# Kernel tuning notes

Measured on AMD Instinct MI355X. Metric: run time of the kernel, lower is better.

Reference implementation:

```python
import jax, jax.numpy as jnp
import numpy as np

B, N_ELEM, N_NODES, E2 = 4096, 2048, 1024, 4096


def setup_inputs() -> dict:
    key = jax.random.key(0)
    k = jax.random.split(key, 7)
    return {
        "EA": jax.random.normal(k[0], (B, N_ELEM), dtype=jnp.float32),
        "e": jax.random.normal(k[1], (B, N_ELEM), dtype=jnp.float32),
        "q": jax.random.normal(k[2], (B, N_NODES, 2), dtype=jnp.float32),
        "r": jax.random.normal(k[3], (B, N_NODES, 2), dtype=jnp.float32),
        "vecs": jax.random.normal(k[4], (E2, 2), dtype=jnp.float32),
        "node_ids": jax.random.randint(k[5], (E2,), 0, N_NODES, dtype=jnp.int32),
        "elem_ids": jax.random.randint(k[6], (E2,), 0, N_ELEM, dtype=jnp.int32),
    }


def reference(EA, e, q, r, vecs, node_ids, elem_ids):
    # axial_forces = EA * e : [B, N_ELEM]
    axial = EA * e
    # gather per incidence entry and scale by the 2-vector: [B, E2, 2]
    contrib = axial[:, elem_ids][..., None] * vecs[None, :, :]
    n_sample, n_nodes = q.shape[0], q.shape[1]
    # scatter-add contributions into per-node residual: [B, N_NODES, 2]
    residual = jnp.zeros((n_sample, n_nodes, 2), dtype=EA.dtype)
    residual = residual.at[:, node_ids, :].add(contrib)
    residual = residual - q - r
    return jnp.mean(jnp.square(residual))
```

## Files before the change

kernel.cpp:

```cpp
#include <hip/hip_runtime.h>

#define B_SAMPLES 4096
#define N_ELEM    2048
#define N_NODES   1024
#define E2        4096
#define BLOCK     256
#define SLOTS     32
#define S         4
#define MAIN_BLOCKS (B_SAMPLES / S)

#define WS_CNT_OFF   0
#define WS_ELL_OFF   4096
#define WS_PART_OFF  (4096 + SLOTS * N_NODES * 16)

__global__ __launch_bounds__(BLOCK) void neq_zero_kernel(
    float4* __restrict__ ell, int* __restrict__ cnt)
{
    const int i = blockIdx.x * BLOCK + threadIdx.x;
    ell[i] = make_float4(0.f, 0.f, 0.f, 0.f);
    if (i < N_NODES) cnt[i] = 0;
}

__global__ __launch_bounds__(BLOCK) void neq_build_kernel(
    const float* __restrict__ vecs, const int* __restrict__ node_ids,
    const int* __restrict__ elem_ids, int* __restrict__ cnt,
    float4* __restrict__ ell)
{
    const int j = blockIdx.x * BLOCK + threadIdx.x;
    int nid = node_ids[j];
    int eid = elem_ids[j];
    float2 v = ((const float2*)vecs)[j];
    int slot = atomicAdd(&cnt[nid], 1);
    if (slot < SLOTS) {
        ell[slot * N_NODES + nid] = make_float4(v.x, v.y, __int_as_float(eid), 0.f);
    }
}

__global__ __launch_bounds__(BLOCK, 4) void neq_main_kernel(
    const float* __restrict__ EA, const float* __restrict__ e,
    const float* __restrict__ q,  const float* __restrict__ r,
    const int* __restrict__ cnt, const float4* __restrict__ ell,
    float* __restrict__ partial)
{
    __shared__ float4 axial4[N_ELEM];
    __shared__ float red[BLOCK / 64];

    const int b0 = blockIdx.x * S;
    const int t = threadIdx.x;

#pragma unroll
    for (int i = 0; i < N_ELEM / BLOCK; ++i) {
        int eid = t + i * BLOCK;
        float4 p;
        const float* EAp = EA + (size_t)b0 * N_ELEM + eid;
        const float* ep  = e  + (size_t)b0 * N_ELEM + eid;
        p.x = EAp[0 * N_ELEM] * ep[0 * N_ELEM];
        p.y = EAp[1 * N_ELEM] * ep[1 * N_ELEM];
        p.z = EAp[2 * N_ELEM] * ep[2 * N_ELEM];
        p.w = EAp[3 * N_ELEM] * ep[3 * N_ELEM];
        axial4[eid] = p;
    }

    int c0 = min(cnt[t], SLOTS);
    int c1 = min(cnt[t + 256], SLOTS);
    int c2 = min(cnt[t + 512], SLOTS);
    int c3 = min(cnt[t + 768], SLOTS);
    int kmax = max(max(c0, c1), max(c2, c3));
    __syncthreads();

    float accx[4][S] = {};
    float accy[4][S] = {};
    for (int k = 0; k < kmax; ++k) {
        const float4* row = ell + k * N_NODES + t;
#pragma unroll
        for (int i = 0; i < 4; ++i) {
            float4 pk = row[i * BLOCK];
            int eid = __float_as_int(pk.z);
            float4 ax = axial4[eid];
            accx[i][0] += ax.x * pk.x;  accy[i][0] += ax.x * pk.y;
            accx[i][1] += ax.y * pk.x;  accy[i][1] += ax.y * pk.y;
            accx[i][2] += ax.z * pk.x;  accy[i][2] += ax.z * pk.y;
            accx[i][3] += ax.w * pk.x;  accy[i][3] += ax.w * pk.y;
        }
    }

    float acc = 0.f;
#pragma unroll
    for (int s = 0; s < S; ++s) {
        const float2* q2 = (const float2*)(q + (size_t)(b0 + s) * N_NODES * 2);
        const float2* r2 = (const float2*)(r + (size_t)(b0 + s) * N_NODES * 2);
#pragma unroll
        for (int i = 0; i < 4; ++i) {
            int n = t + i * BLOCK;
            float2 qv = q2[n];
            float2 rv = r2[n];
            float x = accx[i][s] - qv.x - rv.x;
            float y = accy[i][s] - qv.y - rv.y;
            acc += x * x + y * y;
        }
    }

#pragma unroll
    for (int off = 32; off > 0; off >>= 1)
        acc += __shfl_down(acc, off, 64);
    if ((t & 63) == 0) red[t >> 6] = acc;
    __syncthreads();
    if (t == 0) partial[blockIdx.x] = red[0] + red[1] + red[2] + red[3];
}

__global__ __launch_bounds__(1024) void neq_reduce_kernel(
    const float* __restrict__ partial, float* __restrict__ out)
{
    __shared__ float red[1024 / 64];
    const int t = threadIdx.x;
    float acc = partial[t];
#pragma unroll
    for (int off = 32; off > 0; off >>= 1)
        acc += __shfl_down(acc, off, 64);
    if ((t & 63) == 0) red[t >> 6] = acc;
    __syncthreads();
    if (t == 0) {
        float s = 0.f;
#pragma unroll
        for (int w = 0; w < 1024 / 64; ++w) s += red[w];
        const float inv_n = 1.0f / (float)((size_t)B_SAMPLES * N_NODES * 2);
        out[0] = s * inv_n;
    }
}

extern "C" void kernel_launch(void* const* d_in, const int* in_sizes, int n_in,
                              void* d_out, int out_size, void* d_ws, size_t ws_size,
                              hipStream_t stream) {
    const float* EA       = (const float*)d_in[0];
    const float* e        = (const float*)d_in[1];
    const float* q        = (const float*)d_in[2];
    const float* r        = (const float*)d_in[3];
    const float* vecs     = (const float*)d_in[4];
    const int*   node_ids = (const int*)d_in[5];
    const int*   elem_ids = (const int*)d_in[6];

    char* ws = (char*)d_ws;
    int*    cnt     = (int*)(ws + WS_CNT_OFF);
    float4* ell     = (float4*)(ws + WS_ELL_OFF);
    float*  partial = (float*)(ws + WS_PART_OFF);

    neq_zero_kernel<<<(SLOTS * N_NODES) / BLOCK, BLOCK, 0, stream>>>(ell, cnt);
    neq_build_kernel<<<E2 / BLOCK, BLOCK, 0, stream>>>(
        vecs, node_ids, elem_ids, cnt, ell);
    neq_main_kernel<<<MAIN_BLOCKS, BLOCK, 0, stream>>>(
        EA, e, q, r, cnt, ell, partial);
    neq_reduce_kernel<<<1, 1024, 0, stream>>>(partial, (float*)d_out);
}
```

Measured before the change: 162.4 us.

## Prefetch q/r and ELL rows early, fold final reduction into atomicAdd

Loads q and r and sums them before the scatter loop so their global latency overlaps the ELL traversal. The ELL loop becomes software-pipelined, fetching the next slot row while the current one is processed. The separate single-block reduce kernel is removed: each main block atomically adds its scaled partial into the output, which is zeroed by a memset. This saves a launch and a dependent tail kernel, at the cost of extra registers and a float atomic whose ordering makes the result nondeterministic.

```diff
diff --git a/kernel.cpp b/kernel.cpp
--- a/kernel.cpp
+++ b/kernel.cpp
@@ -11,7 +11,6 @@
 
 #define WS_CNT_OFF   0
 #define WS_ELL_OFF   4096
-#define WS_PART_OFF  (4096 + SLOTS * N_NODES * 16)
 
 __global__ __launch_bounds__(BLOCK) void neq_zero_kernel(
     float4* __restrict__ ell, int* __restrict__ cnt)
@@ -40,7 +39,7 @@
     const float* __restrict__ EA, const float* __restrict__ e,
     const float* __restrict__ q,  const float* __restrict__ r,
     const int* __restrict__ cnt, const float4* __restrict__ ell,
-    float* __restrict__ partial)
+    float* __restrict__ out)
 {
     __shared__ float4 axial4[N_ELEM];
     __shared__ float red[BLOCK / 64];
@@ -61,6 +60,20 @@
         axial4[eid] = p;
     }
 
+    float2 qr[S][4];
+#pragma unroll
+    for (int s = 0; s < S; ++s) {
+        const float2* q2 = (const float2*)(q + (size_t)(b0 + s) * N_NODES * 2);
+        const float2* r2 = (const float2*)(r + (size_t)(b0 + s) * N_NODES * 2);
+#pragma unroll
+        for (int i = 0; i < 4; ++i) {
+            int n = t + i * BLOCK;
+            float2 qv = q2[n];
+            float2 rv = r2[n];
+            qr[s][i] = make_float2(qv.x + rv.x, qv.y + rv.y);
+        }
+    }
+
     int c0 = min(cnt[t], SLOTS);
     int c1 = min(cnt[t + 256], SLOTS);
     int c2 = min(cnt[t + 512], SLOTS);
@@ -70,32 +83,36 @@
 
     float accx[4][S] = {};
     float accy[4][S] = {};
-    for (int k = 0; k < kmax; ++k) {
-        const float4* row = ell + k * N_NODES + t;
+    if (kmax > 0) {
+        float4 pk[4];
 #pragma unroll
-        for (int i = 0; i < 4; ++i) {
-            float4 pk = row[i * BLOCK];
-            int eid = __float_as_int(pk.z);
-            float4 ax = axial4[eid];
-            accx[i][0] += ax.x * pk.x;  accy[i][0] += ax.x * pk.y;
-            accx[i][1] += ax.y * pk.x;  accy[i][1] += ax.y * pk.y;
-            accx[i][2] += ax.z * pk.x;  accy[i][2] += ax.z * pk.y;
-            accx[i][3] += ax.w * pk.x;  accy[i][3] += ax.w * pk.y;
+        for (int i = 0; i < 4; ++i) pk[i] = ell[t + i * BLOCK];
+        for (int k = 0; k < kmax; ++k) {
+            float4 nx[4];
+            const float4* nrow = ell + min(k + 1, SLOTS - 1) * N_NODES + t;
+#pragma unroll
+            for (int i = 0; i < 4; ++i) nx[i] = nrow[i * BLOCK];
+#pragma unroll
+            for (int i = 0; i < 4; ++i) {
+                int eid = __float_as_int(pk[i].z);
+                float4 ax = axial4[eid];
+                accx[i][0] += ax.x * pk[i].x;  accy[i][0] += ax.x * pk[i].y;
+                accx[i][1] += ax.y * pk[i].x;  accy[i][1] += ax.y * pk[i].y;
+                accx[i][2] += ax.z * pk[i].x;  accy[i][2] += ax.z * pk[i].y;
+                accx[i][3] += ax.w * pk[i].x;  accy[i][3] += ax.w * pk[i].y;
+            }
+#pragma unroll
+            for (int i = 0; i < 4; ++i) pk[i] = nx[i];
         }
     }
 
     float acc = 0.f;
 #pragma unroll
     for (int s = 0; s < S; ++s) {
-        const float2* q2 = (const float2*)(q + (size_t)(b0 + s) * N_NODES * 2);
-        const float2* r2 = (const float2*)(r + (size_t)(b0 + s) * N_NODES * 2);
 #pragma unroll
         for (int i = 0; i < 4; ++i) {
-            int n = t + i * BLOCK;
-            float2 qv = q2[n];
-            float2 rv = r2[n];
-            float x = accx[i][s] - qv.x - rv.x;
-            float y = accy[i][s] - qv.y - rv.y;
+            float x = accx[i][s] - qr[s][i].x;
+            float y = accy[i][s] - qr[s][i].y;
             acc += x * x + y * y;
         }
     }
@@ -105,26 +122,9 @@
         acc += __shfl_down(acc, off, 64);
     if ((t & 63) == 0) red[t >> 6] = acc;
     __syncthreads();
-    if (t == 0) partial[blockIdx.x] = red[0] + red[1] + red[2] + red[3];
-}
-
-__global__ __launch_bounds__(1024) void neq_reduce_kernel(
-    const float* __restrict__ partial, float* __restrict__ out)
-{
-    __shared__ float red[1024 / 64];
-    const int t = threadIdx.x;
-    float acc = partial[t];
-#pragma unroll
-    for (int off = 32; off > 0; off >>= 1)
-        acc += __shfl_down(acc, off, 64);
-    if ((t & 63) == 0) red[t >> 6] = acc;
-    __syncthreads();
     if (t == 0) {
-        float s = 0.f;
-#pragma unroll
-        for (int w = 0; w < 1024 / 64; ++w) s += red[w];
         const float inv_n = 1.0f / (float)((size_t)B_SAMPLES * N_NODES * 2);
-        out[0] = s * inv_n;
+        atomicAdd(out, (red[0] + red[1] + red[2] + red[3]) * inv_n);
     }
 }
 
@@ -140,14 +140,14 @@
     const int*   elem_ids = (const int*)d_in[6];
 
     char* ws = (char*)d_ws;
-    int*    cnt     = (int*)(ws + WS_CNT_OFF);
-    float4* ell     = (float4*)(ws + WS_ELL_OFF);
-    float*  partial = (float*)(ws + WS_PART_OFF);
+    int*    cnt = (int*)(ws + WS_CNT_OFF);
+    float4* ell = (float4*)(ws + WS_ELL_OFF);
+
+    hipMemsetAsync(d_out, 0, sizeof(float), stream);
 
     neq_zero_kernel<<<(SLOTS * N_NODES) / BLOCK, BLOCK, 0, stream>>>(ell, cnt);
     neq_build_kernel<<<E2 / BLOCK, BLOCK, 0, stream>>>(
         vecs, node_ids, elem_ids, cnt, ell);
     neq_main_kernel<<<MAIN_BLOCKS, BLOCK, 0, stream>>>(
-        EA, e, q, r, cnt, ell, partial);
-    neq_reduce_kernel<<<1, 1024, 0, stream>>>(partial, (float*)d_out);
+        EA, e, q, r, cnt, ell, (float*)d_out);
 }
```

Measured after the change: 177.3 us. 1.09x slower.

## Use 512-thread main blocks, per-node slot bounds, and atomic final reduction

Applied to the files above, without the earlier changes.

The main kernel now runs 512 threads per block, so each thread owns two nodes instead of four. The gather loop skips slots beyond each node's own count rather than walking every row up to the block-wide maximum. The separate reduce kernel and partial buffer are dropped: each block atomically adds its scaled sum into the output, which is zeroed with a memset first. This removes a kernel launch and spreads the gather over more threads, at the cost of a branch inside the loop, a float atomicAdd whose summation order is not fixed, and a different occupancy, since __launch_bounds__(BLOCK,4) now means 512 threads with 32KB of LDS per block.

```diff
diff --git a/kernel.cpp b/kernel.cpp
--- a/kernel.cpp
+++ b/kernel.cpp
@@ -4,29 +4,29 @@
 #define N_ELEM    2048
 #define N_NODES   1024
 #define E2        4096
-#define BLOCK     256
+#define BLOCK     512
 #define SLOTS     32
 #define S         4
+#define NPT       (N_NODES / BLOCK)
 #define MAIN_BLOCKS (B_SAMPLES / S)
 
 #define WS_CNT_OFF   0
 #define WS_ELL_OFF   4096
-#define WS_PART_OFF  (4096 + SLOTS * N_NODES * 16)
 
-__global__ __launch_bounds__(BLOCK) void neq_zero_kernel(
+__global__ __launch_bounds__(256) void neq_zero_kernel(
     float4* __restrict__ ell, int* __restrict__ cnt)
 {
-    const int i = blockIdx.x * BLOCK + threadIdx.x;
+    const int i = blockIdx.x * 256 + threadIdx.x;
     ell[i] = make_float4(0.f, 0.f, 0.f, 0.f);
     if (i < N_NODES) cnt[i] = 0;
 }
 
-__global__ __launch_bounds__(BLOCK) void neq_build_kernel(
+__global__ __launch_bounds__(256) void neq_build_kernel(
     const float* __restrict__ vecs, const int* __restrict__ node_ids,
     const int* __restrict__ elem_ids, int* __restrict__ cnt,
     float4* __restrict__ ell)
 {
-    const int j = blockIdx.x * BLOCK + threadIdx.x;
+    const int j = blockIdx.x * 256 + threadIdx.x;
     int nid = node_ids[j];
     int eid = elem_ids[j];
     float2 v = ((const float2*)vecs)[j];
@@ -40,7 +40,7 @@
     const float* __restrict__ EA, const float* __restrict__ e,
     const float* __restrict__ q,  const float* __restrict__ r,
     const int* __restrict__ cnt, const float4* __restrict__ ell,
-    float* __restrict__ partial)
+    float* __restrict__ out)
 {
     __shared__ float4 axial4[N_ELEM];
     __shared__ float red[BLOCK / 64];
@@ -62,25 +62,26 @@
     }
 
     int c0 = min(cnt[t], SLOTS);
-    int c1 = min(cnt[t + 256], SLOTS);
-    int c2 = min(cnt[t + 512], SLOTS);
-    int c3 = min(cnt[t + 768], SLOTS);
-    int kmax = max(max(c0, c1), max(c2, c3));
+    int c1 = min(cnt[t + BLOCK], SLOTS);
+    int kmax = max(c0, c1);
     __syncthreads();
 
-    float accx[4][S] = {};
-    float accy[4][S] = {};
+    float accx[NPT][S] = {};
+    float accy[NPT][S] = {};
     for (int k = 0; k < kmax; ++k) {
         const float4* row = ell + k * N_NODES + t;
 #pragma unroll
-        for (int i = 0; i < 4; ++i) {
-            float4 pk = row[i * BLOCK];
-            int eid = __float_as_int(pk.z);
-            float4 ax = axial4[eid];
-            accx[i][0] += ax.x * pk.x;  accy[i][0] += ax.x * pk.y;
-            accx[i][1] += ax.y * pk.x;  accy[i][1] += ax.y * pk.y;
-            accx[i][2] += ax.z * pk.x;  accy[i][2] += ax.z * pk.y;
-            accx[i][3] += ax.w * pk.x;  accy[i][3] += ax.w * pk.y;
+        for (int i = 0; i < NPT; ++i) {
+            int ci = (i == 0) ? c0 : c1;
+            if (k < ci) {
+                float4 pk = row[i * BLOCK];
+                int eid = __float_as_int(pk.z);
+                float4 ax = axial4[eid];
+                accx[i][0] += ax.x * pk.x;  accy[i][0] += ax.x * pk.y;
+                accx[i][1] += ax.y * pk.x;  accy[i][1] += ax.y * pk.y;
+                accx[i][2] += ax.z * pk.x;  accy[i][2] += ax.z * pk.y;
+                accx[i][3] += ax.w * pk.x;  accy[i][3] += ax.w * pk.y;
+            }
         }
     }
 
@@ -90,7 +91,7 @@
         const float2* q2 = (const float2*)(q + (size_t)(b0 + s) * N_NODES * 2);
         const float2* r2 = (const float2*)(r + (size_t)(b0 + s) * N_NODES * 2);
 #pragma unroll
-        for (int i = 0; i < 4; ++i) {
+        for (int i = 0; i < NPT; ++i) {
             int n = t + i * BLOCK;
             float2 qv = q2[n];
             float2 rv = r2[n];
@@ -105,26 +106,12 @@
         acc += __shfl_down(acc, off, 64);
     if ((t & 63) == 0) red[t >> 6] = acc;
     __syncthreads();
-    if (t == 0) partial[blockIdx.x] = red[0] + red[1] + red[2] + red[3];
-}
-
-__global__ __launch_bounds__(1024) void neq_reduce_kernel(
-    const float* __restrict__ partial, float* __restrict__ out)
-{
-    __shared__ float red[1024 / 64];
-    const int t = threadIdx.x;
-    float acc = partial[t];
-#pragma unroll
-    for (int off = 32; off > 0; off >>= 1)
-        acc += __shfl_down(acc, off, 64);
-    if ((t & 63) == 0) red[t >> 6] = acc;
-    __syncthreads();
     if (t == 0) {
         float s = 0.f;
 #pragma unroll
-        for (int w = 0; w < 1024 / 64; ++w) s += red[w];
+        for (int w = 0; w < BLOCK / 64; ++w) s += red[w];
         const float inv_n = 1.0f / (float)((size_t)B_SAMPLES * N_NODES * 2);
-        out[0] = s * inv_n;
+        atomicAdd(out, s * inv_n);
     }
 }
 
@@ -140,14 +127,14 @@
     const int*   elem_ids = (const int*)d_in[6];
 
     char* ws = (char*)d_ws;
-    int*    cnt     = (int*)(ws + WS_CNT_OFF);
-    float4* ell     = (float4*)(ws + WS_ELL_OFF);
-    float*  partial = (float*)(ws + WS_PART_OFF);
+    int*    cnt = (int*)(ws + WS_CNT_OFF);
+    float4* ell = (float4*)(ws + WS_ELL_OFF);
 
-    neq_zero_kernel<<<(SLOTS * N_NODES) / BLOCK, BLOCK, 0, stream>>>(ell, cnt);
-    neq_build_kernel<<<E2 / BLOCK, BLOCK, 0, stream>>>(
+    hipMemsetAsync(d_out, 0, sizeof(float), stream);
+
+    neq_zero_kernel<<<(SLOTS * N_NODES) / 256, 256, 0, stream>>>(ell, cnt);
+    neq_build_kernel<<<E2 / 256, 256, 0, stream>>>(
         vecs, node_ids, elem_ids, cnt, ell);
     neq_main_kernel<<<MAIN_BLOCKS, BLOCK, 0, stream>>>(
-        EA, e, q, r, cnt, ell, partial);
-    neq_reduce_kernel<<<1, 1024, 0, stream>>>(partial, (float*)d_out);
+        EA, e, q, r, cnt, ell, (float*)d_out);
 }
```

New measurement: 166.6 us. 2.5% more time.
